# Kernel optimization log

Hardware: AMD Instinct MI355X
Metric: run time of the kernel (lower is better)

## Reference

```python
import jax, jax.numpy as jnp
import numpy as np

B, S, D, H = 2, 2048, 1024, 16
HD = D // H
SCALE = float(np.sqrt(HD))


def setup_inputs() -> dict:
    key = jax.random.key(0)
    k_x, k_wqkv, k_bqkv, k_wo, k_bo = jax.random.split(key, 5)
    std = 1.0 / np.sqrt(D)
    x = jax.random.normal(k_x, (B, S, D), dtype=jnp.float32)
    mask = jnp.tril(jnp.ones((S, S), dtype=jnp.int32))[None, None]  # (1,1,S,S) causal
    W_qkv = jax.random.normal(k_wqkv, (D, 3 * D), dtype=jnp.float32) * std
    b_qkv = jax.random.normal(k_bqkv, (3 * D,), dtype=jnp.float32) * std
    W_o = jax.random.normal(k_wo, (D, D), dtype=jnp.float32) * std
    b_o = jax.random.normal(k_bo, (D,), dtype=jnp.float32) * std
    return {"x": x, "W_qkv": W_qkv, "b_qkv": b_qkv, "W_o": W_o, "b_o": b_o, "mask": mask}


def reference(x, W_qkv, b_qkv, W_o, b_o, mask):
    # fused QKV projection: (B,S,3D) -> (3,B,H,S,HD)
    qkv = x @ W_qkv + b_qkv
    qkv = qkv.reshape(B, S, 3, H, HD).transpose(2, 0, 3, 1, 4)
    Q, K, V = qkv[0], qkv[1], qkv[2]
    # scaled dot-product attention with explicit mask
    scores = jnp.einsum('bhqd,bhkd->bhqk', Q, K) / SCALE
    scores = jnp.where(mask == 0, -jnp.inf, scores)
    attn = jax.nn.softmax(scores, axis=-1)  # dropout p=0.0 -> identity
    context = jnp.einsum('bhqk,bhkd->bhqd', attn, V)
    context = context.transpose(0, 2, 1, 3).reshape(B, S, D)
    return context @ W_o + b_o
```

## Files before the change

kernel.cpp:

```cpp
#include <hip/hip_runtime.h>
#include <hip/hip_bf16.h>
#include <stdint.h>

#define DEV __device__ __forceinline__

typedef __bf16 bf16x8 __attribute__((ext_vector_type(8)));
typedef float f32x4 __attribute__((ext_vector_type(4)));
typedef float f32x16 __attribute__((ext_vector_type(16)));
typedef unsigned short ushort8 __attribute__((ext_vector_type(8)));

DEV uint16_t f2bf(float f) {
  uint32_t u = __float_as_uint(f);
  u += 0x7fffu + ((u >> 16) & 1u);
  return (uint16_t)(u >> 16);
}

DEV float exp2r(float x) {
  float r;
  asm("v_exp_f32 %0, %1" : "=v"(r) : "v"(x));
  return r;
}

DEV void gload_lds16(const void* g, void* l) {
  __builtin_amdgcn_global_load_lds(
      (const __attribute__((address_space(1))) void*)g,
      (__attribute__((address_space(3))) void*)l, 16, 0, 0);
}

DEV void swap32u(uint32_t& a, uint32_t& b) {
#if defined(__has_builtin) && __has_builtin(__builtin_amdgcn_permlane32_swap)
  auto r = __builtin_amdgcn_permlane32_swap(a, b, false, false);
  a = (uint32_t)r[0];
  b = (uint32_t)r[1];
#else
  uint32_t as = __shfl_xor(a, 32), bs = __shfl_xor(b, 32);
  uint32_t na = (threadIdx.x & 32) ? bs : a;
  uint32_t nb = (threadIdx.x & 32) ? b : as;
  a = na; b = nb;
#endif
}
DEV void swap32f(float& a, float& b) {
  uint32_t ua = __float_as_uint(a), ub = __float_as_uint(b);
  swap32u(ua, ub);
  a = __uint_as_float(ua); b = __uint_as_float(ub);
}

__global__ __launch_bounds__(256) void k_prep(const float* __restrict__ W0,
                                              uint16_t* __restrict__ WT0,
                                              const float* __restrict__ W1,
                                              uint16_t* __restrict__ WT1,
                                              const float* __restrict__ X,
                                              uint16_t* __restrict__ Xb) {
  const int z = blockIdx.z;
  const int tid = threadIdx.x;
  if (z == 2) {
    const int nt4 = 1048576, stride = 48 * 16 * 256;
    int base = (blockIdx.y * 48 + blockIdx.x) * 256 + tid;
    for (int i = base; i < nt4; i += stride) {
      float4 v = *reinterpret_cast<const float4*>(X + (size_t)i * 4);
      ushort4 o = { f2bf(v.x), f2bf(v.y), f2bf(v.z), f2bf(v.w) };
      *reinterpret_cast<ushort4*>(Xb + (size_t)i * 4) = o;
    }
    return;
  }
  if (z == 1 && blockIdx.x >= 16) return;
  const float* W = z ? W1 : W0;
  uint16_t* WT = z ? WT1 : WT0;
  const int K = 1024, N = z ? 1024 : 3072;
  __shared__ float t[64][65];
  int n0 = blockIdx.x * 64, k0 = blockIdx.y * 64;
  int r = tid >> 4, c4 = (tid & 15) * 4;
#pragma unroll
  for (int p = 0; p < 4; ++p) {
    int kr = p * 16 + r;
    float4 v = *reinterpret_cast<const float4*>(W + (size_t)(k0 + kr) * N + n0 + c4);
    t[kr][c4] = v.x; t[kr][c4 + 1] = v.y; t[kr][c4 + 2] = v.z; t[kr][c4 + 3] = v.w;
  }
  __syncthreads();
#pragma unroll
  for (int p = 0; p < 4; ++p) {
    int nr = p * 16 + r;
    ushort4 o = { f2bf(t[c4][nr]), f2bf(t[c4 + 1][nr]), f2bf(t[c4 + 2][nr]), f2bf(t[c4 + 3][nr]) };
    *reinterpret_cast<ushort4*>(WT + (size_t)(n0 + nr) * K + k0 + c4) = o;
  }
}

__global__ __launch_bounds__(256, 2) void k_gemm0(const uint16_t* __restrict__ A,
                                                  const uint16_t* __restrict__ Bw,
                                                  const float* __restrict__ bias,
                                                  uint16_t* __restrict__ o0,
                                                  uint16_t* __restrict__ o1,
                                                  uint16_t* __restrict__ o2) {
  constexpr int K = 1024;
  __shared__ __attribute__((aligned(16))) char SMEM[65536];
  const int tid = threadIdx.x;
  const int lane = tid & 63, wid = tid >> 6;
  const int g = lane >> 4, c = lane & 15;
  const int nb = gridDim.x * gridDim.y;
  const int bid = blockIdx.y * gridDim.x + blockIdx.x;
  const int cpx = nb >> 3;
  const int swz = (bid & 7) * cpx + (bid >> 3);
  const int bx = swz % gridDim.x, by = swz / gridDim.x;
  const int row0 = by * 128, col0 = bx * 128;
  const int wrow = (wid >> 1) * 64, wcol = (wid & 1) * 64;
  f32x4 acc[4][4] = {};
  const uint16_t* Ag = A + (size_t)row0 * K;
  const uint16_t* Bg = Bw + (size_t)col0 * K;

  const int srow = tid >> 3;
  const int ssw = ((tid & 7) ^ (srow & 7)) * 8;
  auto stageAB = [&](int t, int buf) {
    const int k0 = t * 64;
    char* ab = SMEM + buf * 16384;
    char* bb = SMEM + 32768 + buf * 16384;
#pragma unroll
    for (int i = 0; i < 4; ++i) {
      int row = i * 32 + srow;
      gload_lds16(Ag + (size_t)row * K + k0 + ssw, ab + i * 4096 + tid * 16);
      gload_lds16(Bg + (size_t)row * K + k0 + ssw, bb + i * 4096 + tid * 16);
    }
  };

  stageAB(0, 0);
  asm volatile("s_waitcnt vmcnt(0)" ::: "memory");
  __builtin_amdgcn_s_barrier();
  asm volatile("" ::: "memory");

  for (int t = 0; t < 16; ++t) {
    if (t + 1 < 16) stageAB(t + 1, (t + 1) & 1);
    const uint16_t* Ac = (const uint16_t*)(SMEM + (t & 1) * 16384);
    const uint16_t* Bc = (const uint16_t*)(SMEM + 32768 + (t & 1) * 16384);
    __builtin_amdgcn_s_setprio(1);
#pragma unroll
    for (int kk = 0; kk < 2; ++kk) {
      bf16x8 af[4], bf[4];
#pragma unroll
      for (int m = 0; m < 4; ++m)
        af[m] = *reinterpret_cast<const bf16x8*>(
            &Ac[(wrow + m * 16 + c) * 64 + (((kk * 4 + g) ^ (c & 7)) << 3)]);
#pragma unroll
      for (int n = 0; n < 4; ++n)
        bf[n] = *reinterpret_cast<const bf16x8*>(
            &Bc[(wcol + n * 16 + c) * 64 + (((kk * 4 + g) ^ (c & 7)) << 3)]);
#pragma unroll
      for (int m = 0; m < 4; ++m)
#pragma unroll
        for (int n = 0; n < 4; ++n)
          acc[m][n] = __builtin_amdgcn_mfma_f32_16x16x32_bf16(af[m], bf[n], acc[m][n], 0, 0, 0);
    }
    __builtin_amdgcn_s_setprio(0);
    asm volatile("s_waitcnt vmcnt(0)" ::: "memory");
    __builtin_amdgcn_s_barrier();
    asm volatile("" ::: "memory");
  }

  if (col0 >= 2048) {
    uint16_t* TB = (uint16_t*)SMEM;
#pragma unroll
    for (int n = 0; n < 4; ++n) {
      int col_l = wcol + n * 16 + c;
      float bs = bias[col0 + col_l];
#pragma unroll
      for (int m = 0; m < 4; ++m)
#pragma unroll
        for (int r = 0; r < 4; ++r) {
          int row_l = wrow + m * 16 + g * 4 + r;
          TB[col_l * 136 + row_l] = f2bf(acc[m][n][r] + bs);
        }
    }
    __syncthreads();
    const int col_l = tid >> 1, half = tid & 1;
    const int d = (col0 - 2048) + col_l;
    const int h = d >> 6, hd = d & 63;
    const int b = row0 >> 11, s0 = row0 & 2047;
    uint16_t* dst = o2 + ((size_t)(b * 16 + h) * 64 + hd) * 2048 + s0 + half * 64;
    const uint16_t* src = &TB[col_l * 136 + half * 64];
#pragma unroll
    for (int k = 0; k < 8; ++k) {
      ushort8 v = *reinterpret_cast<const ushort8*>(src + k * 8);
      *reinterpret_cast<ushort8*>(dst + k * 8) = v;
    }
  } else {
#pragma unroll
    for (int m = 0; m < 4; ++m) {
#pragma unroll
      for (int n = 0; n < 4; ++n) {
        int col = col0 + wcol + n * 16 + c;
        float bs = bias[col];
#pragma unroll
        for (int r = 0; r < 4; ++r) {
          int row = row0 + wrow + m * 16 + g * 4 + r;
          float v = acc[m][n][r] + bs;
          int which = col >> 10, d = col & 1023, h = d >> 6, hd = d & 63;
          int b = row >> 11, s = row & 2047;
          int bh = b * 16 + h;
          if (which == 0)      o0[((size_t)bh * 2048 + s) * 64 + hd] = f2bf(v * 0.1803368801111244f);
          else                 o1[((size_t)bh * 2048 + s) * 64 + hd] = f2bf(v);
        }
      }
    }
  }
}

__global__ __launch_bounds__(256, 2) void k_gemm1(const uint16_t* __restrict__ A,
                                                  const uint16_t* __restrict__ Bw,
                                                  const float* __restrict__ bias,
                                                  float* __restrict__ of) {
  constexpr int K = 1024;
  __shared__ __attribute__((aligned(16))) char SMEM[49152];
  const int tid = threadIdx.x;
  const int lane = tid & 63, wid = tid >> 6;
  const int g = lane >> 4, c = lane & 15;
  const int nb = gridDim.x * gridDim.y;
  const int bid = blockIdx.y * gridDim.x + blockIdx.x;
  const int cpx = nb >> 3;
  const int swz = (bid & 7) * cpx + (bid >> 3);
  const int bx = swz % gridDim.x, by = swz / gridDim.x;
  const int row0 = by * 128, col0 = bx * 64;
  f32x4 acc[2][4] = {};
  const uint16_t* Ag = A + (size_t)row0 * K;
  const uint16_t* Bg = Bw + (size_t)col0 * K;

  const int srow = tid >> 3;
  const int ssw = ((tid & 7) ^ (srow & 7)) * 8;
  auto stageAB = [&](int t, int buf) {
    const int k0 = t * 64;
    char* ab = SMEM + buf * 16384;
    char* bb = SMEM + 32768 + buf * 8192;
#pragma unroll
    for (int i = 0; i < 4; ++i)
      gload_lds16(Ag + (size_t)(i * 32 + srow) * K + k0 + ssw, ab + i * 4096 + tid * 16);
#pragma unroll
    for (int i = 0; i < 2; ++i)
      gload_lds16(Bg + (size_t)(i * 32 + srow) * K + k0 + ssw, bb + i * 4096 + tid * 16);
  };

  stageAB(0, 0);
  asm volatile("s_waitcnt vmcnt(0)" ::: "memory");
  __builtin_amdgcn_s_barrier();
  asm volatile("" ::: "memory");

  for (int t = 0; t < 16; ++t) {
    if (t + 1 < 16) stageAB(t + 1, (t + 1) & 1);
    const uint16_t* Ac = (const uint16_t*)(SMEM + (t & 1) * 16384);
    const uint16_t* Bc = (const uint16_t*)(SMEM + 32768 + (t & 1) * 8192);
    __builtin_amdgcn_s_setprio(1);
#pragma unroll
    for (int kk = 0; kk < 2; ++kk) {
      bf16x8 af[2], bf[4];
#pragma unroll
      for (int m = 0; m < 2; ++m)
        af[m] = *reinterpret_cast<const bf16x8*>(
            &Ac[(wid * 32 + m * 16 + c) * 64 + (((kk * 4 + g) ^ (c & 7)) << 3)]);
#pragma unroll
      for (int n = 0; n < 4; ++n)
        bf[n] = *reinterpret_cast<const bf16x8*>(
            &Bc[(n * 16 + c) * 64 + (((kk * 4 + g) ^ (c & 7)) << 3)]);
#pragma unroll
      for (int m = 0; m < 2; ++m)
#pragma unroll
        for (int n = 0; n < 4; ++n)
          acc[m][n] = __builtin_amdgcn_mfma_f32_16x16x32_bf16(af[m], bf[n], acc[m][n], 0, 0, 0);
    }
    __builtin_amdgcn_s_setprio(0);
    asm volatile("s_waitcnt vmcnt(0)" ::: "memory");
    __builtin_amdgcn_s_barrier();
    asm volatile("" ::: "memory");
  }

#pragma unroll
  for (int m = 0; m < 2; ++m) {
#pragma unroll
    for (int n = 0; n < 4; ++n) {
      int col = col0 + n * 16 + c;
      float bs = bias[col];
#pragma unroll
      for (int r = 0; r < 4; ++r) {
        int row = row0 + wid * 32 + m * 16 + g * 4 + r;
        of[(size_t)row * 1024 + col] = acc[m][n][r] + bs;
      }
    }
  }
}

__global__ __launch_bounds__(512, 4) void k_attn(const uint16_t* __restrict__ Qb,
                                                 const uint16_t* __restrict__ Kb,
                                                 const uint16_t* __restrict__ Vb,
                                                 uint16_t* __restrict__ ctx) {
  __shared__ __attribute__((aligned(16))) char SMEM[65536];
  uint16_t* Ksb = (uint16_t*)SMEM;
  uint16_t* Vsb = (uint16_t*)(SMEM + 32768);
  const int bid = blockIdx.x;
  const int xcd = bid & 7;
  const int idx = bid >> 3;
  const int bh = 4 * xcd + (idx & 3);
  const int jj = idx >> 2;
  const int qt = (idx < 32) ? (15 - jj) : (jj - 8);
  const int tid = threadIdx.x, lane = tid & 63, wid = tid >> 6;
  const int qw = wid & 3, kw = wid >> 2;
  const int h2 = lane >> 5, c = lane & 31;
  const int q0 = qt * 128;
  const int qi = q0 + qw * 32 + c;
  const int nt = qt + 1;
  const uint16_t* Qh = Qb + (size_t)bh * 2048 * 64;
  const uint16_t* Kh = Kb + (size_t)bh * 2048 * 64;
  const uint16_t* Vh = Vb + (size_t)bh * 64 * 2048;

  bf16x8 qf[4];
#pragma unroll
  for (int kk = 0; kk < 4; ++kk)
    qf[kk] = *reinterpret_cast<const bf16x8*>(&Qh[(size_t)qi * 64 + kk * 16 + h2 * 8]);

  float m_ = -1e30f, l_ = 0.f;
  f32x16 oT0 = {}, oT1 = {};

  const int srow = tid >> 3;
  const int ssw = ((tid & 7) ^ (srow & 7)) * 8;
  const int vr = tid >> 4;
  const int vsw = ((tid & 15) ^ (vr & 15)) * 8;
  auto stage = [&](int T, int buf) {
    const int j0 = T * 128;
    char* kb = (char*)(Ksb + buf * 8192);
    char* vb = (char*)(Vsb + buf * 8192);
#pragma unroll
    for (int i = 0; i < 2; ++i)
      gload_lds16(Kh + (size_t)(j0 + i * 64 + srow) * 64 + ssw, kb + i * 8192 + tid * 16);
#pragma unroll
    for (int i = 0; i < 2; ++i)
      gload_lds16(Vh + (size_t)(i * 32 + vr) * 2048 + j0 + vsw, vb + i * 8192 + tid * 16);
  };

  union U4 { uint32_t u[4]; bf16x8 v; };

  stage(0, 0);
  asm volatile("s_waitcnt vmcnt(0)" ::: "memory");
  __builtin_amdgcn_s_barrier();
  asm volatile("" ::: "memory");

  for (int T = 0; T < nt; ++T) {
    const int j0 = T * 128;
    if (T + 1 < nt) stage(T + 1, (T + 1) & 1);
    const uint16_t* Kc = Ksb + (T & 1) * 8192;
    const uint16_t* Vc = Vsb + (T & 1) * 8192;
    f32x16 s0 = {}, s1 = {};
    __builtin_amdgcn_s_setprio(1);
#pragma unroll
    for (int kk = 0; kk < 4; ++kk) {
      const int off = ((kk * 2 + h2) ^ (c & 7)) << 3;
      bf16x8 k0 = *reinterpret_cast<const bf16x8*>(&Kc[(kw * 64 + c) * 64 + off]);
      bf16x8 k1 = *reinterpret_cast<const bf16x8*>(&Kc[(kw * 64 + 32 + c) * 64 + off]);
      s0 = __builtin_amdgcn_mfma_f32_32x32x16_bf16(k0, qf[kk], s0, 0, 0, 0);
      s1 = __builtin_amdgcn_mfma_f32_32x32x16_bf16(k1, qf[kk], s1, 0, 0, 0);
    }
    __builtin_amdgcn_s_setprio(0);
    if (T == qt) {
#pragma unroll
      for (int r = 0; r < 16; ++r) {
        int key0 = j0 + kw * 64 + (r & 3) + 8 * (r >> 2) + 4 * h2;
        if (key0 > qi) s0[r] = -INFINITY;
        if (key0 + 32 > qi) s1[r] = -INFINITY;
      }
    }
    float tm[16];
#pragma unroll
    for (int r = 0; r < 16; ++r)
      tm[r] = fmaxf(s0[r], s1[r]);
#pragma unroll
    for (int s = 8; s >= 1; s >>= 1)
#pragma unroll
      for (int r = 0; r < s; ++r) tm[r] = fmaxf(tm[r], tm[r + s]);
    float xa = tm[0], xb = tm[0];
    swap32f(xa, xb);
    float mx = fmaxf(xa, xb);
    bool nogrow = __all(mx <= m_ + 8.0f) != 0;
    float nm = m_, scl = 1.0f;
    if (!nogrow) { nm = fmaxf(m_, mx); scl = exp2r(m_ - nm); m_ = nm; }
    float sum = 0.f;
    uint32_t W[16];
#pragma unroll
    for (int w = 0; w < 8; ++w) {
      float a0 = exp2r(s0[2 * w] - nm), a1 = exp2r(s0[2 * w + 1] - nm);
      float b0 = exp2r(s1[2 * w] - nm), b1 = exp2r(s1[2 * w + 1] - nm);
      sum += (a0 + a1) + (b0 + b1);
      asm("v_cvt_pk_bf16_f32 %0, %1, %2" : "=v"(W[w])     : "v"(a0), "v"(a1));
      asm("v_cvt_pk_bf16_f32 %0, %1, %2" : "=v"(W[8 + w]) : "v"(b0), "v"(b1));
    }
    float sa = sum, sb = sum;
    swap32f(sa, sb);
    sum = sa + sb;
    l_ = l_ * scl + sum;
    if (!nogrow) {
#pragma unroll
      for (int r = 0; r < 16; ++r) { oT0[r] *= scl; oT1[r] *= scl; }
    }
#pragma unroll
    for (int cc = 0; cc < 2; ++cc) {
      uint32_t* Wc = &W[cc * 8];
      U4 p0, p1;
      uint32_t a0 = Wc[0], b0 = Wc[2];  swap32u(a0, b0);
      uint32_t a1 = Wc[1], b1 = Wc[3];  swap32u(a1, b1);
      p0.u[0] = a0; p0.u[1] = a1; p0.u[2] = b0; p0.u[3] = b1;
      uint32_t a2 = Wc[4], b2 = Wc[6];  swap32u(a2, b2);
      uint32_t a3 = Wc[5], b3 = Wc[7];  swap32u(a3, b3);
      p1.u[0] = a2; p1.u[1] = a3; p1.u[2] = b2; p1.u[3] = b3;
      const int cb = (kw * 2 + cc) * 4 + h2;
      const int vsl0 = (cb ^ (c & 15)) << 3;
      const int vsl1 = (((cb + 2) & 15) ^ (c & 15)) << 3;
      __builtin_amdgcn_s_setprio(1);
      {
        bf16x8 v0 = *reinterpret_cast<const bf16x8*>(&Vc[c * 128 + vsl0]);
        bf16x8 v1 = *reinterpret_cast<const bf16x8*>(&Vc[c * 128 + vsl1]);
        oT0 = __builtin_amdgcn_mfma_f32_32x32x16_bf16(v0, p0.v, oT0, 0, 0, 0);
        oT0 = __builtin_amdgcn_mfma_f32_32x32x16_bf16(v1, p1.v, oT0, 0, 0, 0);
      }
      {
        bf16x8 v0 = *reinterpret_cast<const bf16x8*>(&Vc[(32 + c) * 128 + vsl0]);
        bf16x8 v1 = *reinterpret_cast<const bf16x8*>(&Vc[(32 + c) * 128 + vsl1]);
        oT1 = __builtin_amdgcn_mfma_f32_32x32x16_bf16(v0, p0.v, oT1, 0, 0, 0);
        oT1 = __builtin_amdgcn_mfma_f32_32x32x16_bf16(v1, p1.v, oT1, 0, 0, 0);
      }
      __builtin_amdgcn_s_setprio(0);
    }
    asm volatile("s_waitcnt vmcnt(0)" ::: "memory");
    __builtin_amdgcn_s_barrier();
    asm volatile("" ::: "memory");
  }

  float* MB = (float*)SMEM;
  float* OB = MB + 512;
  const int sl = qw * 64 + lane;
  if (kw == 1) {
    MB[sl * 2] = m_;
    MB[sl * 2 + 1] = l_;
    float* ob = OB + sl * 33;
#pragma unroll
    for (int r = 0; r < 16; ++r) { ob[r] = oT0[r]; ob[16 + r] = oT1[r]; }
  }
  __syncthreads();
  if (kw == 0) {
    float mB = MB[sl * 2], lB = MB[sl * 2 + 1];
    const float* ob = OB + sl * 33;
    float m = fmaxf(m_, mB);
    float eA = exp2r(m_ - m), eB = exp2r(mB - m);
    float inv = 1.0f / (l_ * eA + lB * eB);
    float sA = eA * inv, sB = eB * inv;
    const int b = bh >> 4, h = bh & 15;
    int token = b * 2048 + qi;
    uint16_t* outp = ctx + (size_t)token * 1024 + h * 64;
#pragma unroll
    for (int hb = 0; hb < 2; ++hb) {
      const f32x16& o = hb ? oT1 : oT0;
#pragma unroll
      for (int q4 = 0; q4 < 4; ++q4) {
        ushort4 w;
        w.x = f2bf(o[q4 * 4 + 0] * sA + ob[hb * 16 + q4 * 4 + 0] * sB);
        w.y = f2bf(o[q4 * 4 + 1] * sA + ob[hb * 16 + q4 * 4 + 1] * sB);
        w.z = f2bf(o[q4 * 4 + 2] * sA + ob[hb * 16 + q4 * 4 + 2] * sB);
        w.w = f2bf(o[q4 * 4 + 3] * sA + ob[hb * 16 + q4 * 4 + 3] * sB);
        *reinterpret_cast<ushort4*>(outp + hb * 32 + 8 * q4 + 4 * h2) = w;
      }
    }
  }
}

extern "C" void kernel_launch(void* const* d_in, const int* in_sizes, int n_in,
                              void* d_out, int out_size, void* d_ws, size_t ws_size,
                              hipStream_t stream) {
  (void)in_sizes; (void)n_in; (void)out_size; (void)ws_size;
  const float* x     = (const float*)d_in[0];
  const float* W_qkv = (const float*)d_in[1];
  const float* b_qkv = (const float*)d_in[2];
  const float* W_o   = (const float*)d_in[3];
  const float* b_o   = (const float*)d_in[4];
  uint16_t* ws    = (uint16_t*)d_ws;
  uint16_t* woT   = ws;
  uint16_t* xb    = woT + 1024 * 1024;
  uint16_t* wqkvT = xb + 4096 * 1024;
  uint16_t* Qb    = wqkvT + 3072 * 1024;
  uint16_t* Kb    = Qb + 32 * 2048 * 64;
  uint16_t* Vb    = Kb + 32 * 2048 * 64;
  uint16_t* ctx   = Vb + 32 * 2048 * 64;

  k_prep<<<dim3(48, 16, 3), 256, 0, stream>>>(W_qkv, wqkvT, W_o, woT, x, xb);
  k_gemm0<<<dim3(24, 32), 256, 0, stream>>>(xb, wqkvT, b_qkv, Qb, Kb, Vb);
  k_attn<<<512, 512, 0, stream>>>(Qb, Kb, Vb, ctx);
  k_gemm1<<<dim3(16, 32), 256, 0, stream>>>(ctx, woT, b_o, (float*)d_out);
}
```

Baseline: 91.36 us.

## Split long causal attention tiles across two blocks with a merge kernel

The heaviest query tiles (qt 10–15) are now split along the KV range into two work items, each handled by its own block, and a table-driven schedule balances them across 704 blocks. Split blocks write unnormalised partial outputs plus max and sum into scratch that reuses the xb buffer, and a new k_merge kernel combines them into bf16 context. This targets the tail imbalance of causal attention. It costs an extra kernel launch and fp32 partial-result traffic.

```diff
diff --git a/kernel.cpp b/kernel.cpp
--- a/kernel.cpp
+++ b/kernel.cpp
@@ -44,6 +44,13 @@
   swap32u(ua, ub);
   a = __uint_as_float(ua); b = __uint_as_float(ub);
 }
+
+__constant__ int QT_TAB[22] = {9, 8, 15, 15, 14, 7, 14, 13, 13, 12, 6,
+                               12, 11, 11, 10, 5, 10, 4, 3, 2, 1, 0};
+__constant__ int T0_TAB[22] = {0, 0, 0, 8, 0, 0, 8, 0, 7, 0, 0,
+                               7, 0, 6, 0, 0, 6, 0, 0, 0, 0, 0};
+__constant__ int T1_TAB[22] = {10, 9, 8, 16, 8, 8, 15, 7, 14, 7, 7,
+                               13, 6, 12, 6, 6, 11, 5, 4, 3, 2, 1};
 
 __global__ __launch_bounds__(256) void k_prep(const float* __restrict__ W0,
                                               uint16_t* __restrict__ WT0,
@@ -286,7 +293,9 @@
 __global__ __launch_bounds__(512, 4) void k_attn(const uint16_t* __restrict__ Qb,
                                                  const uint16_t* __restrict__ Kb,
                                                  const uint16_t* __restrict__ Vb,
-                                                 uint16_t* __restrict__ ctx) {
+                                                 uint16_t* __restrict__ ctx,
+                                                 float* __restrict__ PO,
+                                                 float* __restrict__ PML) {
   __shared__ __attribute__((aligned(16))) char SMEM[65536];
   uint16_t* Ksb = (uint16_t*)SMEM;
   uint16_t* Vsb = (uint16_t*)(SMEM + 32768);
@@ -294,14 +303,14 @@
   const int xcd = bid & 7;
   const int idx = bid >> 3;
   const int bh = 4 * xcd + (idx & 3);
-  const int jj = idx >> 2;
-  const int qt = (idx < 32) ? (15 - jj) : (jj - 8);
+  const int j = idx >> 2;
+  const int qt = QT_TAB[j];
+  const int T0 = T0_TAB[j], T1 = T1_TAB[j];
   const int tid = threadIdx.x, lane = tid & 63, wid = tid >> 6;
   const int qw = wid & 3, kw = wid >> 2;
   const int h2 = lane >> 5, c = lane & 31;
   const int q0 = qt * 128;
   const int qi = q0 + qw * 32 + c;
-  const int nt = qt + 1;
   const uint16_t* Qh = Qb + (size_t)bh * 2048 * 64;
   const uint16_t* Kh = Kb + (size_t)bh * 2048 * 64;
   const uint16_t* Vh = Vb + (size_t)bh * 64 * 2048;
@@ -332,16 +341,17 @@
 
   union U4 { uint32_t u[4]; bf16x8 v; };
 
-  stage(0, 0);
+  stage(T0, 0);
   asm volatile("s_waitcnt vmcnt(0)" ::: "memory");
   __builtin_amdgcn_s_barrier();
   asm volatile("" ::: "memory");
 
-  for (int T = 0; T < nt; ++T) {
+  for (int T = T0; T < T1; ++T) {
     const int j0 = T * 128;
-    if (T + 1 < nt) stage(T + 1, (T + 1) & 1);
-    const uint16_t* Kc = Ksb + (T & 1) * 8192;
-    const uint16_t* Vc = Vsb + (T & 1) * 8192;
+    const int buf = (T - T0) & 1;
+    if (T + 1 < T1) stage(T + 1, buf ^ 1);
+    const uint16_t* Kc = Ksb + buf * 8192;
+    const uint16_t* Vc = Vsb + buf * 8192;
     f32x16 s0 = {}, s1 = {};
     __builtin_amdgcn_s_setprio(1);
 #pragma unroll
@@ -442,24 +452,79 @@
     const float* ob = OB + sl * 33;
     float m = fmaxf(m_, mB);
     float eA = exp2r(m_ - m), eB = exp2r(mB - m);
-    float inv = 1.0f / (l_ * eA + lB * eB);
-    float sA = eA * inv, sB = eB * inv;
-    const int b = bh >> 4, h = bh & 15;
-    int token = b * 2048 + qi;
-    uint16_t* outp = ctx + (size_t)token * 1024 + h * 64;
-#pragma unroll
-    for (int hb = 0; hb < 2; ++hb) {
-      const f32x16& o = hb ? oT1 : oT0;
-#pragma unroll
-      for (int q4 = 0; q4 < 4; ++q4) {
-        ushort4 w;
-        w.x = f2bf(o[q4 * 4 + 0] * sA + ob[hb * 16 + q4 * 4 + 0] * sB);
-        w.y = f2bf(o[q4 * 4 + 1] * sA + ob[hb * 16 + q4 * 4 + 1] * sB);
-        w.z = f2bf(o[q4 * 4 + 2] * sA + ob[hb * 16 + q4 * 4 + 2] * sB);
-        w.w = f2bf(o[q4 * 4 + 3] * sA + ob[hb * 16 + q4 * 4 + 3] * sB);
-        *reinterpret_cast<ushort4*>(outp + hb * 32 + 8 * q4 + 4 * h2) = w;
-      }
-    }
+    float l = l_ * eA + lB * eB;
+    if (T1 - T0 == qt + 1) {
+      float inv = 1.0f / l;
+      float sA = eA * inv, sB = eB * inv;
+      const int b = bh >> 4, h = bh & 15;
+      int token = b * 2048 + qi;
+      uint16_t* outp = ctx + (size_t)token * 1024 + h * 64;
+#pragma unroll
+      for (int hb = 0; hb < 2; ++hb) {
+        const f32x16& o = hb ? oT1 : oT0;
+#pragma unroll
+        for (int q4 = 0; q4 < 4; ++q4) {
+          ushort4 w;
+          w.x = f2bf(o[q4 * 4 + 0] * sA + ob[hb * 16 + q4 * 4 + 0] * sB);
+          w.y = f2bf(o[q4 * 4 + 1] * sA + ob[hb * 16 + q4 * 4 + 1] * sB);
+          w.z = f2bf(o[q4 * 4 + 2] * sA + ob[hb * 16 + q4 * 4 + 2] * sB);
+          w.w = f2bf(o[q4 * 4 + 3] * sA + ob[hb * 16 + q4 * 4 + 3] * sB);
+          *reinterpret_cast<ushort4*>(outp + hb * 32 + 8 * q4 + 4 * h2) = w;
+        }
+      }
+    } else {
+      const int half = (T0 != 0) ? 1 : 0;
+      const int slot = (bh * 6 + (qt - 10)) * 2 + half;
+      float* po = PO + (size_t)slot * 8192;
+      float* pml = PML + (size_t)slot * 256;
+      const int row_l = qw * 32 + c;
+      pml[row_l * 2] = m;
+      pml[row_l * 2 + 1] = l;
+#pragma unroll
+      for (int hb = 0; hb < 2; ++hb) {
+        const f32x16& o = hb ? oT1 : oT0;
+#pragma unroll
+        for (int q4 = 0; q4 < 4; ++q4) {
+          float4 w = { o[q4 * 4 + 0] * eA + ob[hb * 16 + q4 * 4 + 0] * eB,
+                       o[q4 * 4 + 1] * eA + ob[hb * 16 + q4 * 4 + 1] * eB,
+                       o[q4 * 4 + 2] * eA + ob[hb * 16 + q4 * 4 + 2] * eB,
+                       o[q4 * 4 + 3] * eA + ob[hb * 16 + q4 * 4 + 3] * eB };
+          *reinterpret_cast<float4*>(po + row_l * 64 + hb * 32 + 8 * q4 + 4 * h2) = w;
+        }
+      }
+    }
+  }
+}
+
+__global__ __launch_bounds__(256) void k_merge(const float* __restrict__ PO,
+                                               const float* __restrict__ PML,
+                                               uint16_t* __restrict__ ctx) {
+  const int bid = blockIdx.x;
+  const int bh = bid & 31, pi = bid >> 5;
+  const int qt = 10 + pi;
+  const int slot0 = (bh * 6 + pi) * 2;
+  const float* poL = PO + (size_t)slot0 * 8192;
+  const float* poH = poL + 8192;
+  const float* mlL = PML + (size_t)slot0 * 256;
+  const float* mlH = mlL + 256;
+  const int t = threadIdx.x;
+  const int r = t >> 1, ho = (t & 1) * 32;
+  float mL = mlL[r * 2], lL = mlL[r * 2 + 1];
+  float mH = mlH[r * 2], lH = mlH[r * 2 + 1];
+  float m = fmaxf(mL, mH);
+  float eL = exp2f(mL - m), eH = exp2f(mH - m);
+  float inv = 1.0f / (lL * eL + lH * eH);
+  float sL = eL * inv, sH = eH * inv;
+  const int b = bh >> 4, h = bh & 15;
+  const int token = b * 2048 + qt * 128 + r;
+  uint16_t* outp = ctx + (size_t)token * 1024 + h * 64 + ho;
+#pragma unroll
+  for (int k4 = 0; k4 < 8; ++k4) {
+    float4 a = *reinterpret_cast<const float4*>(poL + r * 64 + ho + k4 * 4);
+    float4 q = *reinterpret_cast<const float4*>(poH + r * 64 + ho + k4 * 4);
+    ushort4 w = { f2bf(a.x * sL + q.x * sH), f2bf(a.y * sL + q.y * sH),
+                  f2bf(a.z * sL + q.z * sH), f2bf(a.w * sL + q.w * sH) };
+    *reinterpret_cast<ushort4*>(outp + k4 * 4) = w;
   }
 }
 
@@ -480,9 +545,12 @@
   uint16_t* Kb    = Qb + 32 * 2048 * 64;
   uint16_t* Vb    = Kb + 32 * 2048 * 64;
   uint16_t* ctx   = Vb + 32 * 2048 * 64;
+  float* PO  = (float*)xb;
+  float* PML = PO + 384 * 8192;
 
   k_prep<<<dim3(48, 16, 3), 256, 0, stream>>>(W_qkv, wqkvT, W_o, woT, x, xb);
   k_gemm0<<<dim3(24, 32), 256, 0, stream>>>(xb, wqkvT, b_qkv, Qb, Kb, Vb);
-  k_attn<<<512, 512, 0, stream>>>(Qb, Kb, Vb, ctx);
+  k_attn<<<704, 512, 0, stream>>>(Qb, Kb, Vb, ctx, PO, PML);
+  k_merge<<<192, 256, 0, stream>>>(PO, PML, ctx);
   k_gemm1<<<dim3(16, 32), 256, 0, stream>>>(ctx, woT, b_o, (float*)d_out);
 }
```

Measured after the change: 95.85 us. 4.9% more time.
